# Kernel optimization log

Hardware: AMD Instinct MI355X
Metric: run time of the kernel (lower is better)

The kernel has to match this reference:

```python
import jax, jax.numpy as jnp
import numpy as np

VOCAB, EMB, SEQ, UNITS, BATCH = 10000, 100, 80, 512, 2048


def setup_inputs() -> dict:
    key = jax.random.key(0)
    ks = jax.random.split(key, 8)
    s = 0.05  # param scale for numerical stability
    return {
        "ids": jax.random.randint(ks[0], (BATCH, SEQ), 0, VOCAB, dtype=jnp.int32),
        "emb": jax.random.normal(ks[1], (VOCAB, EMB), jnp.float32) * s,
        "W1": jax.random.normal(ks[2], (EMB, 4 * UNITS), jnp.float32) * s,
        "U1": jax.random.normal(ks[3], (UNITS, 4 * UNITS), jnp.float32) * s,
        "b1": jnp.zeros((4 * UNITS,), jnp.float32),
        "W2": jax.random.normal(ks[4], (UNITS, 4 * UNITS), jnp.float32) * s,
        "U2": jax.random.normal(ks[5], (UNITS, 4 * UNITS), jnp.float32) * s,
        "b2": jnp.zeros((4 * UNITS,), jnp.float32),
        "Wd": jax.random.normal(ks[6], (UNITS, 1), jnp.float32) * s,
        "bd": jnp.zeros((1,), jnp.float32),
    }


def _lstm(x, W, U, b):
    # x: [B,T,D]; Keras gate order i,f,g,o; returns (all h [B,T,U], last h [B,U])
    B = x.shape[0]
    H = U.shape[0]
    h0 = jnp.zeros((B, H), x.dtype)

    def step(carry, xt):
        h, c = carry
        z = xt @ W + h @ U + b  # [B,4H]
        i, f, g, o = jnp.split(z, 4, axis=-1)
        c = jax.nn.sigmoid(f) * c + jax.nn.sigmoid(i) * jnp.tanh(g)
        h = jax.nn.sigmoid(o) * jnp.tanh(c)
        return (h, c), h

    (hT, _), hs = jax.lax.scan(step, (h0, h0), jnp.swapaxes(x, 0, 1))
    return jnp.swapaxes(hs, 0, 1), hT


def reference(ids, emb, W1, U1, b1, W2, U2, b2, Wd, bd):
    x = emb[ids]                       # [B,T,EMB]
    x, _ = _lstm(x, W1, U1, b1)        # return_sequences=True -> [B,T,U]
    _, h = _lstm(x, W2, U2, b2)        # last hidden state [B,U]
    logits = h @ Wd + bd               # Dense(1) head
    return jax.nn.sigmoid(logits)      # [B,1]
```

## Files before the change

kernel.cpp:

```cpp
#include <hip/hip_runtime.h>
#include <hip/hip_bf16.h>
#include <math.h>

#define BATCH 2048
#define SEQ   80
#define EMBD  100
#define HU    512
#define NG    2048

typedef short bf16x8 __attribute__((ext_vector_type(8)));
typedef float f32x4  __attribute__((ext_vector_type(4)));

#define AS1(p) ((const __attribute__((address_space(1))) void*)(p))
#define AS3(p) ((__attribute__((address_space(3))) void*)(p))

__device__ __forceinline__ float sigm(float x){ return 1.f/(1.f+__expf(-x)); }


__global__ __launch_bounds__(256) void prep_emb(const float* __restrict__ emb,
                                                __hip_bfloat16* __restrict__ embp)
{
    int idx = blockIdx.x*256 + threadIdx.x;
    int row = idx >> 7, k = idx & 127;
    float v = (k < EMBD) ? emb[row*EMBD + k] : 0.f;
    embp[idx] = __float2bfloat16(v);
}

__global__ __launch_bounds__(256) void prep_wt(
    const float* __restrict__ W1, const float* __restrict__ U1, const float* __restrict__ b1,
    const float* __restrict__ W2, const float* __restrict__ U2, const float* __restrict__ b2,
    __hip_bfloat16* __restrict__ wt1, __hip_bfloat16* __restrict__ wt2,
    float* __restrict__ bp1, float* __restrict__ bp2)
{
    const int n = blockIdx.x;
    const int u = n >> 2, g = n & 3, col = g*HU + u;
    if (blockIdx.y == 0) {
        for (int k = threadIdx.x; k < 640; k += 256) {
            float v = (k < EMBD) ? W1[k*NG + col] : ((k < 128) ? 0.f : U1[(k-128)*NG + col]);
            wt1[n*640 + k] = __float2bfloat16(v);
        }
        if (threadIdx.x == 0) bp1[n] = b1[col];
    } else {
        for (int k = threadIdx.x; k < 1024; k += 256) {
            float v = (k < HU) ? W2[k*NG + col] : U2[(k-HU)*NG + col];
            wt2[n*1024 + k] = __float2bfloat16(v);
        }
        if (threadIdx.x == 0) bp2[n] = b2[col];
    }
}

__global__ __launch_bounds__(512, 4) void round_k(
    const int* __restrict__ ids, const int r,
    const __hip_bfloat16* __restrict__ embp,
    const __hip_bfloat16* __restrict__ wt1, const float* __restrict__ bp1,
    const __hip_bfloat16* __restrict__ wt2, const float* __restrict__ bp2,
    const __hip_bfloat16* __restrict__ h1prev, __hip_bfloat16* __restrict__ h1out,
    const __hip_bfloat16* __restrict__ h2prev, __hip_bfloat16* __restrict__ h2out,
    float* __restrict__ c1, float* __restrict__ c2,
    const int mode)
{
    __shared__ unsigned short As[2][128*64];
    __shared__ unsigned short Bs[2][128*64];

    const int tid  = threadIdx.x;
    const int w    = tid >> 6;
    const int lane = tid & 63;
    const int wM   = w >> 1;
    const int wN   = w & 1;
    const int m0   = blockIdx.y * 128;
    const int n0   = blockIdx.x * 128;

    const bool isL1 = (mode == 1) || (mode == 0 && blockIdx.z == 1);
    const int t     = isL1 ? r : (r - 1);
    const int KTOT  = isL1 ? 640 : 1024;
    const int K1P   = isL1 ? 128 : 512;
    const __hip_bfloat16* wt    = isL1 ? wt1 : wt2;
    const float*          bp    = isL1 ? bp1 : bp2;
    float*                cst   = isL1 ? c1  : c2;
    const __hip_bfloat16* hprev = isL1 ? h1prev : h2prev;
    const __hip_bfloat16* xs    = h1prev;
    __hip_bfloat16*       hout  = isL1 ? h1out : h2out;

    const int rA = lane & 15;
    const int tq = lane >> 4;

    const int rowA = m0 + w*16 + rA;
    const int rowB = n0 + w*16 + rA;
    int myid = 0;
    if (isL1) myid = ids[rowA*SEQ + t];

    f32x4 acc[2][4];
    #pragma unroll
    for (int mi = 0; mi < 2; ++mi)
        #pragma unroll
        for (int ni = 0; ni < 4; ++ni)
            acc[mi][ni] = (f32x4){0.f,0.f,0.f,0.f};

    auto stage = [&](int kt, int buf){
        const int k0 = kt * 64;
        #pragma unroll
        for (int j = 0; j < 2; ++j) {
            const int kk = k0 + (j*4 + tq)*8;
            const __hip_bfloat16* bx = isL1 ? (embp + (size_t)myid*128)
                                            : (xs + (size_t)rowA*HU);
            const __hip_bfloat16* gpA = (kk < K1P)
                ? (bx + kk)
                : (hprev + (size_t)rowA*HU + (kk - K1P));
            __builtin_amdgcn_global_load_lds(AS1(gpA), AS3(&As[buf][w*1024 + j*512]), 16, 0, 0);
            const __hip_bfloat16* gpB = wt + (size_t)rowB*KTOT + kk;
            __builtin_amdgcn_global_load_lds(AS1(gpB), AS3(&Bs[buf][w*1024 + j*512]), 16, 0, 0);
        }
    };

    stage(0, 0);
    __syncthreads();

    const int NT = KTOT / 64;
    for (int kt = 0; kt < NT; ++kt) {
        const int buf = kt & 1;
        if (kt + 1 < NT) stage(kt + 1, buf ^ 1);

        #pragma unroll
        for (int s = 0; s < 2; ++s) {
            bf16x8 aF[2], bF[4];
            #pragma unroll
            for (int mi = 0; mi < 2; ++mi)
                aF[mi] = *(const bf16x8*)&As[buf][(wM*2+mi)*1024 + (s*4+tq)*128 + rA*8];
            #pragma unroll
            for (int ni = 0; ni < 4; ++ni)
                bF[ni] = *(const bf16x8*)&Bs[buf][(wN*4+ni)*1024 + (s*4+tq)*128 + rA*8];
            #pragma unroll
            for (int mi = 0; mi < 2; ++mi)
                #pragma unroll
                for (int ni = 0; ni < 4; ++ni)
                    acc[mi][ni] = __builtin_amdgcn_mfma_f32_16x16x32_bf16(aF[mi], bF[ni], acc[mi][ni], 0, 0, 0);
        }
        __syncthreads();
    }

    const int gq = lane & 3;
    const bool isT = (gq == 2);
    #pragma unroll
    for (int ni = 0; ni < 4; ++ni) {
        const int n  = n0 + wN*64 + ni*16 + (lane & 15);
        const float bv = bp[n];
        const int u  = n >> 2;
        #pragma unroll
        for (int mi = 0; mi < 2; ++mi) {
            #pragma unroll
            for (int rr = 0; rr < 4; ++rr) {
                const int bM = m0 + wM*32 + mi*16 + (lane >> 4)*4 + rr;
                const float z  = acc[mi][ni][rr] + bv;
                const float zz = isT ? 2.f*z : z;
                const float sg = 1.f/(1.f + __expf(-zz));
                const float act = isT ? fmaf(2.f, sg, -1.f) : sg;
                const float act2 = __shfl_xor(act, 2);
                const float pig  = act * act2;
                const float pig1 = __shfl_xor(pig, 1);
                const float c_old = cst[bM*HU + u];
                const float cn  = fmaf(act, c_old, pig1);
                const float tcn = fmaf(2.f, 1.f/(1.f + __expf(-2.f*cn)), -1.f);
                const float tcn2 = __shfl_xor(tcn, 2);
                const float hv  = act * tcn2;
                if (gq == 1) cst[bM*HU + u] = cn;
                else if (gq == 3) hout[bM*HU + u] = __float2bfloat16(hv);
            }
        }
    }
}

__global__ __launch_bounds__(256) void head_k(const __hip_bfloat16* __restrict__ h2,
    const float* __restrict__ Wd, const float* __restrict__ bd, float* __restrict__ out)
{
    const int b = blockIdx.x*4 + (threadIdx.x >> 6);
    const int lane = threadIdx.x & 63;
    float s = 0.f;
    #pragma unroll
    for (int u = lane; u < HU; u += 64) s += __bfloat162float(h2[b*HU + u]) * Wd[u];
    #pragma unroll
    for (int off = 32; off > 0; off >>= 1) s += __shfl_xor(s, off);
    if (lane == 0) out[b] = 1.f/(1.f + __expf(-(s + bd[0])));
}

extern "C" void kernel_launch(void* const* d_in, const int* in_sizes, int n_in,
                              void* d_out, int out_size, void* d_ws, size_t ws_size,
                              hipStream_t stream)
{
    const int*   ids = (const int*)  d_in[0];
    const float* emb = (const float*)d_in[1];
    const float* W1  = (const float*)d_in[2];
    const float* U1  = (const float*)d_in[3];
    const float* b1  = (const float*)d_in[4];
    const float* W2  = (const float*)d_in[5];
    const float* U2  = (const float*)d_in[6];
    const float* b2  = (const float*)d_in[7];
    const float* Wd  = (const float*)d_in[8];
    const float* bd  = (const float*)d_in[9];
    float* out = (float*)d_out;

    char* p = (char*)d_ws;
    __hip_bfloat16* embp = (__hip_bfloat16*)p; p += (size_t)10000*128*2;
    __hip_bfloat16* wt1  = (__hip_bfloat16*)p; p += (size_t)2048*640*2;
    __hip_bfloat16* wt2  = (__hip_bfloat16*)p; p += (size_t)2048*1024*2;
    float* bp1 = (float*)p; p += 2048*4;
    float* bp2 = (float*)p; p += 2048*4;

    char* state = p;
    const size_t HS = (size_t)BATCH*HU;
    __hip_bfloat16* h1[2]; __hip_bfloat16* h2[2];
    h1[0] = (__hip_bfloat16*)p; p += HS*2;
    h1[1] = (__hip_bfloat16*)p; p += HS*2;
    h2[0] = (__hip_bfloat16*)p; p += HS*2;
    h2[1] = (__hip_bfloat16*)p; p += HS*2;
    float* c1 = (float*)p; p += HS*4;
    float* c2 = (float*)p; p += HS*4;

    hipMemsetAsync(state, 0, HS*(4*2 + 2*4), stream);

    prep_emb<<<10000*128/256, 256, 0, stream>>>(emb, embp);
    prep_wt<<<dim3(2048,2), 256, 0, stream>>>(W1,U1,b1,W2,U2,b2, wt1,wt2,bp1,bp2);

    for (int r = 0; r <= SEQ; ++r) {
        const int mode = (r == 0) ? 1 : ((r == SEQ) ? 2 : 0);
        dim3 g(16, 16, (mode == 0) ? 2 : 1);
        const int cur = r & 1, prv = cur ^ 1;
        round_k<<<g, 512, 0, stream>>>(ids, r, embp, wt1, bp1, wt2, bp2,
                                       h1[prv], h1[cur], h2[prv], h2[cur], c1, c2, mode);
    }
    head_k<<<BATCH/4, 256, 0, stream>>>(h2[0], Wd, bd, out);
}
```

Baseline: 3.200 ms.

## Fuse all LSTM time steps into one persistent kernel with a grid barrier

Replaces the 81 per-step kernel launches with a single persistent kernel of 256 blocks. Each block runs the layer-1 step and then the layer-2 step for its tile, and a global atomic barrier separates time steps. The cell state now lives in LDS for the whole sequence instead of being read and written in global memory every step. This removes launch overhead and the cell-state traffic. In exchange it relies on all 256 blocks being resident at once for the barrier to work, and it runs the two layers one after the other inside each block instead of as separate blocks in parallel.

```diff
diff --git a/kernel.cpp b/kernel.cpp
--- a/kernel.cpp
+++ b/kernel.cpp
@@ -7,14 +7,13 @@
 #define EMBD  100
 #define HU    512
 #define NG    2048
+#define NBLK  256
 
 typedef short bf16x8 __attribute__((ext_vector_type(8)));
 typedef float f32x4  __attribute__((ext_vector_type(4)));
 
 #define AS1(p) ((const __attribute__((address_space(1))) void*)(p))
 #define AS3(p) ((__attribute__((address_space(3))) void*)(p))
-
-__device__ __forceinline__ float sigm(float x){ return 1.f/(1.f+__expf(-x)); }
 
 
 __global__ __launch_bounds__(256) void prep_emb(const float* __restrict__ emb,
@@ -49,45 +48,51 @@
     }
 }
 
-__global__ __launch_bounds__(512, 4) void round_k(
-    const int* __restrict__ ids, const int r,
-    const __hip_bfloat16* __restrict__ embp,
-    const __hip_bfloat16* __restrict__ wt1, const float* __restrict__ bp1,
-    const __hip_bfloat16* __restrict__ wt2, const float* __restrict__ bp2,
-    const __hip_bfloat16* __restrict__ h1prev, __hip_bfloat16* __restrict__ h1out,
-    const __hip_bfloat16* __restrict__ h2prev, __hip_bfloat16* __restrict__ h2out,
-    float* __restrict__ c1, float* __restrict__ c2,
-    const int mode)
-{
-    __shared__ unsigned short As[2][128*64];
-    __shared__ unsigned short Bs[2][128*64];
-
+__device__ __forceinline__ void gbar(unsigned* cnt, unsigned* gen)
+{
+    __syncthreads();
+    if (threadIdx.x == 0) {
+        __threadfence();
+        unsigned g = __hip_atomic_load(gen, __ATOMIC_RELAXED, __HIP_MEMORY_SCOPE_AGENT);
+        unsigned a = __hip_atomic_fetch_add(cnt, 1u, __ATOMIC_ACQ_REL, __HIP_MEMORY_SCOPE_AGENT);
+        if (a == NBLK - 1u) {
+            __hip_atomic_store(cnt, 0u, __ATOMIC_RELAXED, __HIP_MEMORY_SCOPE_AGENT);
+            __hip_atomic_fetch_add(gen, 1u, __ATOMIC_ACQ_REL, __HIP_MEMORY_SCOPE_AGENT);
+        } else {
+            while (__hip_atomic_load(gen, __ATOMIC_RELAXED, __HIP_MEMORY_SCOPE_AGENT) == g)
+                __builtin_amdgcn_s_sleep(2);
+        }
+        __threadfence();
+    }
+    __syncthreads();
+}
+
+template<int KTOT, int K1P, bool GATHER>
+__device__ __forceinline__ void layer_step(
+    const int* __restrict__ ids, const int t,
+    const __hip_bfloat16* __restrict__ xs,
+    const __hip_bfloat16* __restrict__ hprev,
+    const __hip_bfloat16* __restrict__ wt,
+    const float* __restrict__ bp,
+    float* __restrict__ csl,
+    __hip_bfloat16* __restrict__ hout,
+    unsigned short* As0, unsigned short* As1,
+    unsigned short* Bs0, unsigned short* Bs1,
+    const int m0, const int n0)
+{
     const int tid  = threadIdx.x;
     const int w    = tid >> 6;
     const int lane = tid & 63;
     const int wM   = w >> 1;
     const int wN   = w & 1;
-    const int m0   = blockIdx.y * 128;
-    const int n0   = blockIdx.x * 128;
-
-    const bool isL1 = (mode == 1) || (mode == 0 && blockIdx.z == 1);
-    const int t     = isL1 ? r : (r - 1);
-    const int KTOT  = isL1 ? 640 : 1024;
-    const int K1P   = isL1 ? 128 : 512;
-    const __hip_bfloat16* wt    = isL1 ? wt1 : wt2;
-    const float*          bp    = isL1 ? bp1 : bp2;
-    float*                cst   = isL1 ? c1  : c2;
-    const __hip_bfloat16* hprev = isL1 ? h1prev : h2prev;
-    const __hip_bfloat16* xs    = h1prev;
-    __hip_bfloat16*       hout  = isL1 ? h1out : h2out;
 
     const int rA = lane & 15;
     const int tq = lane >> 4;
-
     const int rowA = m0 + w*16 + rA;
     const int rowB = n0 + w*16 + rA;
-    int myid = 0;
-    if (isL1) myid = ids[rowA*SEQ + t];
+
+    const __hip_bfloat16* bx = GATHER ? (xs + (size_t)ids[rowA*SEQ + t]*128)
+                                      : (xs + (size_t)rowA*HU);
 
     f32x4 acc[2][4];
     #pragma unroll
@@ -97,27 +102,29 @@
             acc[mi][ni] = (f32x4){0.f,0.f,0.f,0.f};
 
     auto stage = [&](int kt, int buf){
+        unsigned short* Ad = (buf ? As1 : As0) + w*1024;
+        unsigned short* Bd = (buf ? Bs1 : Bs0) + w*1024;
         const int k0 = kt * 64;
         #pragma unroll
         for (int j = 0; j < 2; ++j) {
             const int kk = k0 + (j*4 + tq)*8;
-            const __hip_bfloat16* bx = isL1 ? (embp + (size_t)myid*128)
-                                            : (xs + (size_t)rowA*HU);
             const __hip_bfloat16* gpA = (kk < K1P)
                 ? (bx + kk)
                 : (hprev + (size_t)rowA*HU + (kk - K1P));
-            __builtin_amdgcn_global_load_lds(AS1(gpA), AS3(&As[buf][w*1024 + j*512]), 16, 0, 0);
+            __builtin_amdgcn_global_load_lds(AS1(gpA), AS3(Ad + j*512), 16, 0, 0);
             const __hip_bfloat16* gpB = wt + (size_t)rowB*KTOT + kk;
-            __builtin_amdgcn_global_load_lds(AS1(gpB), AS3(&Bs[buf][w*1024 + j*512]), 16, 0, 0);
+            __builtin_amdgcn_global_load_lds(AS1(gpB), AS3(Bd + j*512), 16, 0, 0);
         }
     };
 
     stage(0, 0);
     __syncthreads();
 
-    const int NT = KTOT / 64;
+    constexpr int NT = KTOT / 64;
     for (int kt = 0; kt < NT; ++kt) {
         const int buf = kt & 1;
+        const unsigned short* Ab = buf ? As1 : As0;
+        const unsigned short* Bb = buf ? Bs1 : Bs0;
         if (kt + 1 < NT) stage(kt + 1, buf ^ 1);
 
         #pragma unroll
@@ -125,10 +132,10 @@
             bf16x8 aF[2], bF[4];
             #pragma unroll
             for (int mi = 0; mi < 2; ++mi)
-                aF[mi] = *(const bf16x8*)&As[buf][(wM*2+mi)*1024 + (s*4+tq)*128 + rA*8];
+                aF[mi] = *(const bf16x8*)&Ab[(wM*2+mi)*1024 + (s*4+tq)*128 + rA*8];
             #pragma unroll
             for (int ni = 0; ni < 4; ++ni)
-                bF[ni] = *(const bf16x8*)&Bs[buf][(wN*4+ni)*1024 + (s*4+tq)*128 + rA*8];
+                bF[ni] = *(const bf16x8*)&Bb[(wN*4+ni)*1024 + (s*4+tq)*128 + rA*8];
             #pragma unroll
             for (int mi = 0; mi < 2; ++mi)
                 #pragma unroll
@@ -142,14 +149,16 @@
     const bool isT = (gq == 2);
     #pragma unroll
     for (int ni = 0; ni < 4; ++ni) {
-        const int n  = n0 + wN*64 + ni*16 + (lane & 15);
+        const int nl = wN*64 + ni*16 + (lane & 15);
+        const int n  = n0 + nl;
         const float bv = bp[n];
-        const int u  = n >> 2;
+        const int ug  = n >> 2;
+        const int ul  = nl >> 2;
         #pragma unroll
         for (int mi = 0; mi < 2; ++mi) {
             #pragma unroll
             for (int rr = 0; rr < 4; ++rr) {
-                const int bM = m0 + wM*32 + mi*16 + (lane >> 4)*4 + rr;
+                const int rowl = wM*32 + mi*16 + (lane >> 4)*4 + rr;
                 const float z  = acc[mi][ni][rr] + bv;
                 const float zz = isT ? 2.f*z : z;
                 const float sg = 1.f/(1.f + __expf(-zz));
@@ -157,15 +166,55 @@
                 const float act2 = __shfl_xor(act, 2);
                 const float pig  = act * act2;
                 const float pig1 = __shfl_xor(pig, 1);
-                const float c_old = cst[bM*HU + u];
+                const float c_old = csl[rowl*33 + ul];
                 const float cn  = fmaf(act, c_old, pig1);
                 const float tcn = fmaf(2.f, 1.f/(1.f + __expf(-2.f*cn)), -1.f);
                 const float tcn2 = __shfl_xor(tcn, 2);
                 const float hv  = act * tcn2;
-                if (gq == 1) cst[bM*HU + u] = cn;
-                else if (gq == 3) hout[bM*HU + u] = __float2bfloat16(hv);
+                if (gq == 1) csl[rowl*33 + ul] = cn;
+                else if (gq == 3) hout[(size_t)(m0 + rowl)*HU + ug] = __float2bfloat16(hv);
             }
         }
+    }
+}
+
+__global__ __launch_bounds__(512, 2) void lstm_persist(
+    const int* __restrict__ ids,
+    const __hip_bfloat16* __restrict__ embp,
+    const __hip_bfloat16* __restrict__ wt1, const float* __restrict__ bp1,
+    const __hip_bfloat16* __restrict__ wt2, const float* __restrict__ bp2,
+    __hip_bfloat16* h1a, __hip_bfloat16* h1b,
+    __hip_bfloat16* h2a, __hip_bfloat16* h2b,
+    unsigned* cnt, unsigned* gen)
+{
+    __shared__ unsigned short As[2][8192];
+    __shared__ unsigned short Bs[2][8192];
+    __shared__ float cs1[128*33];
+    __shared__ float cs2[128*33];
+
+    const int bid = blockIdx.x;
+    const int uB  = (bid & 7)*2 + ((bid >> 3) & 1);
+    const int rB  = bid >> 4;
+    const int m0  = rB * 128;
+    const int n0  = uB * 128;
+
+    for (int i = threadIdx.x; i < 128*33; i += 512) { cs1[i] = 0.f; cs2[i] = 0.f; }
+
+    for (int r = 0; r <= SEQ; ++r) {
+        const int ip = (r - 1) & 1;
+        const int ic = r & 1;
+        const __hip_bfloat16* h1p = ip ? h1b : h1a;
+        __hip_bfloat16*       h1c = ic ? h1b : h1a;
+        const __hip_bfloat16* h2c = ic ? h2b : h2a;
+        __hip_bfloat16*       h2p = ip ? h2b : h2a;
+
+        if (r < SEQ)
+            layer_step<640,128,true>(ids, r, embp, h1p, wt1, bp1, cs1, h1c,
+                                     &As[0][0], &As[1][0], &Bs[0][0], &Bs[1][0], m0, n0);
+        if (r >= 1)
+            layer_step<1024,512,false>(nullptr, 0, h1p, h2c, wt2, bp2, cs2, h2p,
+                                     &As[0][0], &As[1][0], &Bs[0][0], &Bs[1][0], m0, n0);
+        gbar(cnt, gen);
     }
 }
 
@@ -198,34 +247,26 @@
     const float* bd  = (const float*)d_in[9];
     float* out = (float*)d_out;
 
+    const size_t HS = (size_t)BATCH*HU;
     char* p = (char*)d_ws;
-    __hip_bfloat16* embp = (__hip_bfloat16*)p; p += (size_t)10000*128*2;
-    __hip_bfloat16* wt1  = (__hip_bfloat16*)p; p += (size_t)2048*640*2;
-    __hip_bfloat16* wt2  = (__hip_bfloat16*)p; p += (size_t)2048*1024*2;
-    float* bp1 = (float*)p; p += 2048*4;
-    float* bp2 = (float*)p; p += 2048*4;
-
-    char* state = p;
-    const size_t HS = (size_t)BATCH*HU;
-    __hip_bfloat16* h1[2]; __hip_bfloat16* h2[2];
-    h1[0] = (__hip_bfloat16*)p; p += HS*2;
-    h1[1] = (__hip_bfloat16*)p; p += HS*2;
-    h2[0] = (__hip_bfloat16*)p; p += HS*2;
-    h2[1] = (__hip_bfloat16*)p; p += HS*2;
-    float* c1 = (float*)p; p += HS*4;
-    float* c2 = (float*)p; p += HS*4;
-
-    hipMemsetAsync(state, 0, HS*(4*2 + 2*4), stream);
+    unsigned* bar = (unsigned*)p;                    p += 256;
+    __hip_bfloat16* h1a = (__hip_bfloat16*)p;        p += HS*2;
+    __hip_bfloat16* h1b = (__hip_bfloat16*)p;        p += HS*2;
+    __hip_bfloat16* h2a = (__hip_bfloat16*)p;        p += HS*2;
+    __hip_bfloat16* h2b = (__hip_bfloat16*)p;        p += HS*2;
+    __hip_bfloat16* embp = (__hip_bfloat16*)p;       p += (size_t)10000*128*2;
+    __hip_bfloat16* wt1  = (__hip_bfloat16*)p;       p += (size_t)2048*640*2;
+    __hip_bfloat16* wt2  = (__hip_bfloat16*)p;       p += (size_t)2048*1024*2;
+    float* bp1 = (float*)p;                          p += 2048*4;
+    float* bp2 = (float*)p;                          p += 2048*4;
+
+    hipMemsetAsync(d_ws, 0, 256 + 4*HS*2, stream);
 
     prep_emb<<<10000*128/256, 256, 0, stream>>>(emb, embp);
     prep_wt<<<dim3(2048,2), 256, 0, stream>>>(W1,U1,b1,W2,U2,b2, wt1,wt2,bp1,bp2);
 
-    for (int r = 0; r <= SEQ; ++r) {
-        const int mode = (r == 0) ? 1 : ((r == SEQ) ? 2 : 0);
-        dim3 g(16, 16, (mode == 0) ? 2 : 1);
-        const int cur = r & 1, prv = cur ^ 1;
-        round_k<<<g, 512, 0, stream>>>(ids, r, embp, wt1, bp1, wt2, bp2,
-                                       h1[prv], h1[cur], h2[prv], h2[cur], c1, c2, mode);
-    }
-    head_k<<<BATCH/4, 256, 0, stream>>>(h2[0], Wd, bd, out);
-}
+    lstm_persist<<<NBLK, 512, 0, stream>>>(ids, embp, wt1, bp1, wt2, bp2,
+                                           h1a, h1b, h2a, h2b, &bar[0], &bar[1]);
+
+    head_k<<<BATCH/4, 256, 0, stream>>>(h2b, Wd, bd, out);
+}
```

Result: slower. 5.621 ms (+75.7%).

## Replace per-timestep launches with persistent LSTM kernel using grid barrier

Applied to the files above, without the earlier changes.

Replaces the 81 per-round kernel launches with one persistent kernel of 256 blocks that loops over all timesteps and synchronizes through a global atomic barrier. Each block owns a fixed 64-row by 256-gate tile, so the cell state stays in registers and no longer goes through global memory. The h1 row tile is staged once into LDS and reused by both layers, and both layers run back-to-back inside a round. This removes launch overhead and cell-state traffic, but relies on all 256 blocks being co-resident, since the spin barrier would deadlock otherwise. The heavier per-block LDS footprint also reduces occupancy.

```diff
diff --git a/kernel.cpp b/kernel.cpp
--- a/kernel.cpp
+++ b/kernel.cpp
@@ -1,29 +1,26 @@
 #include <hip/hip_runtime.h>
 #include <hip/hip_bf16.h>
-#include <math.h>
 
 #define BATCH 2048
 #define SEQ   80
 #define EMBD  100
 #define HU    512
 #define NG    2048
+#define NBLK  256
 
 typedef short bf16x8 __attribute__((ext_vector_type(8)));
 typedef float f32x4  __attribute__((ext_vector_type(4)));
+typedef int   i32x4  __attribute__((ext_vector_type(4)));
 
 #define AS1(p) ((const __attribute__((address_space(1))) void*)(p))
 #define AS3(p) ((__attribute__((address_space(3))) void*)(p))
 
-__device__ __forceinline__ float sigm(float x){ return 1.f/(1.f+__expf(-x)); }
-
-
 __global__ __launch_bounds__(256) void prep_emb(const float* __restrict__ emb,
                                                 __hip_bfloat16* __restrict__ embp)
 {
     int idx = blockIdx.x*256 + threadIdx.x;
     int row = idx >> 7, k = idx & 127;
-    float v = (k < EMBD) ? emb[row*EMBD + k] : 0.f;
-    embp[idx] = __float2bfloat16(v);
+    embp[idx] = __float2bfloat16(k < EMBD ? emb[row*EMBD + k] : 0.f);
 }
 
 __global__ __launch_bounds__(256) void prep_wt(
@@ -49,123 +46,222 @@
     }
 }
 
-__global__ __launch_bounds__(512, 4) void round_k(
-    const int* __restrict__ ids, const int r,
+__global__ __launch_bounds__(512, 2) void lstm_persist(
+    const int* __restrict__ ids,
     const __hip_bfloat16* __restrict__ embp,
     const __hip_bfloat16* __restrict__ wt1, const float* __restrict__ bp1,
     const __hip_bfloat16* __restrict__ wt2, const float* __restrict__ bp2,
-    const __hip_bfloat16* __restrict__ h1prev, __hip_bfloat16* __restrict__ h1out,
-    const __hip_bfloat16* __restrict__ h2prev, __hip_bfloat16* __restrict__ h2out,
-    float* __restrict__ c1, float* __restrict__ c2,
-    const int mode)
-{
-    __shared__ unsigned short As[2][128*64];
-    __shared__ unsigned short Bs[2][128*64];
-
-    const int tid  = threadIdx.x;
-    const int w    = tid >> 6;
-    const int lane = tid & 63;
-    const int wM   = w >> 1;
-    const int wN   = w & 1;
-    const int m0   = blockIdx.y * 128;
-    const int n0   = blockIdx.x * 128;
-
-    const bool isL1 = (mode == 1) || (mode == 0 && blockIdx.z == 1);
-    const int t     = isL1 ? r : (r - 1);
-    const int KTOT  = isL1 ? 640 : 1024;
-    const int K1P   = isL1 ? 128 : 512;
-    const __hip_bfloat16* wt    = isL1 ? wt1 : wt2;
-    const float*          bp    = isL1 ? bp1 : bp2;
-    float*                cst   = isL1 ? c1  : c2;
-    const __hip_bfloat16* hprev = isL1 ? h1prev : h2prev;
-    const __hip_bfloat16* xs    = h1prev;
-    __hip_bfloat16*       hout  = isL1 ? h1out : h2out;
-
-    const int rA = lane & 15;
-    const int tq = lane >> 4;
-
-    const int rowA = m0 + w*16 + rA;
-    const int rowB = n0 + w*16 + rA;
-    int myid = 0;
-    if (isL1) myid = ids[rowA*SEQ + t];
-
+    __hip_bfloat16* __restrict__ h1a, __hip_bfloat16* __restrict__ h1b,
+    __hip_bfloat16* __restrict__ h2a, __hip_bfloat16* __restrict__ h2b,
+    unsigned long long* bar)
+{
+    __shared__ __align__(16) unsigned short hx[64*520];
+    __shared__ __align__(16) unsigned short Bs[2][16384];
+    __shared__ __align__(16) unsigned short sb[2][4096];
+
+    const int tid = threadIdx.x;
+    const int w = tid >> 6, lane = tid & 63;
+    const int l15 = lane & 15, tq = lane >> 4;
+    const int wM = w >> 2, wN = w & 3;
+    const int uB = blockIdx.x & 7, rB = blockIdx.x >> 3;
+    const int m0 = rB * 64, n0 = uB * 256;
+
+    float c1r[4][2][4] = {};
+    float c2r[4][2][4] = {};
     f32x4 acc[2][4];
-    #pragma unroll
-    for (int mi = 0; mi < 2; ++mi)
+
+    auto zacc = [&](){
+        #pragma unroll
+        for (int mi = 0; mi < 2; ++mi)
+            #pragma unroll
+            for (int ni = 0; ni < 4; ++ni)
+                acc[mi][ni] = (f32x4){0.f,0.f,0.f,0.f};
+    };
+
+    auto stageB = [&](const __hip_bfloat16* wt, int KTOT, int kt, unsigned short* Bd){
+        const int k0 = kt * 64;
+        #pragma unroll
+        for (int cc = 0; cc < 2; ++cc) {
+            const int chunk = w*2 + cc;
+            #pragma unroll
+            for (int j = 0; j < 2; ++j) {
+                const __hip_bfloat16* gp = wt + (size_t)(n0 + chunk*16 + l15)*KTOT
+                                              + k0 + (j*4 + tq)*8;
+                __builtin_amdgcn_global_load_lds(AS1(gp), AS3(Bd + chunk*1024 + j*512), 16, 0, 0);
+            }
+        }
+    };
+
+    auto afragS = [&](const unsigned short* S, int s, int mi) -> bf16x8 {
+        return *(const bf16x8*)&S[(wM*2 + mi)*1024 + (s*4 + tq)*128 + l15*8];
+    };
+    auto afragH = [&](int kb, int s, int mi) -> bf16x8 {
+        const int row = wM*32 + mi*16 + l15;
+        const int kp  = kb + s*32 + tq*8;
+        return *(const bf16x8*)((const char*)hx + row*1040 + kp*2);
+    };
+    auto mma2 = [&](bf16x8 a0, bf16x8 a1, const unsigned short* Bb, int s){
+        bf16x8 bF[4];
         #pragma unroll
         for (int ni = 0; ni < 4; ++ni)
-            acc[mi][ni] = (f32x4){0.f,0.f,0.f,0.f};
-
-    auto stage = [&](int kt, int buf){
-        const int k0 = kt * 64;
-        #pragma unroll
-        for (int j = 0; j < 2; ++j) {
-            const int kk = k0 + (j*4 + tq)*8;
-            const __hip_bfloat16* bx = isL1 ? (embp + (size_t)myid*128)
-                                            : (xs + (size_t)rowA*HU);
-            const __hip_bfloat16* gpA = (kk < K1P)
-                ? (bx + kk)
-                : (hprev + (size_t)rowA*HU + (kk - K1P));
-            __builtin_amdgcn_global_load_lds(AS1(gpA), AS3(&As[buf][w*1024 + j*512]), 16, 0, 0);
-            const __hip_bfloat16* gpB = wt + (size_t)rowB*KTOT + kk;
-            __builtin_amdgcn_global_load_lds(AS1(gpB), AS3(&Bs[buf][w*1024 + j*512]), 16, 0, 0);
-        }
-    };
-
-    stage(0, 0);
-    __syncthreads();
-
-    const int NT = KTOT / 64;
-    for (int kt = 0; kt < NT; ++kt) {
-        const int buf = kt & 1;
-        if (kt + 1 < NT) stage(kt + 1, buf ^ 1);
-
-        #pragma unroll
-        for (int s = 0; s < 2; ++s) {
-            bf16x8 aF[2], bF[4];
-            #pragma unroll
-            for (int mi = 0; mi < 2; ++mi)
-                aF[mi] = *(const bf16x8*)&As[buf][(wM*2+mi)*1024 + (s*4+tq)*128 + rA*8];
-            #pragma unroll
-            for (int ni = 0; ni < 4; ++ni)
-                bF[ni] = *(const bf16x8*)&Bs[buf][(wN*4+ni)*1024 + (s*4+tq)*128 + rA*8];
-            #pragma unroll
-            for (int mi = 0; mi < 2; ++mi)
+            bF[ni] = *(const bf16x8*)&Bb[(wN*4 + ni)*1024 + (s*4 + tq)*128 + l15*8];
+        #pragma unroll
+        for (int ni = 0; ni < 4; ++ni) {
+            acc[0][ni] = __builtin_amdgcn_mfma_f32_16x16x32_bf16(a0, bF[ni], acc[0][ni], 0, 0, 0);
+            acc[1][ni] = __builtin_amdgcn_mfma_f32_16x16x32_bf16(a1, bF[ni], acc[1][ni], 0, 0, 0);
+        }
+    };
+
+    auto sbwrite = [&](unsigned short* S, i32x4 v){
+        const int row = tid >> 3, t8 = tid & 7;
+        *(i32x4*)((char*)S + ((row >> 4)*1024 + t8*128 + (row & 15)*8)*2) = v;
+    };
+    auto hxwrite = [&](i32x4* hr){
+        #pragma unroll
+        for (int t = 0; t < 8; ++t)
+            *(i32x4*)((char*)hx + (t*8 + (tid >> 6))*1040 + (tid & 63)*16) = hr[t];
+    };
+
+    auto epilogue = [&](const float* bp, float (&cr)[4][2][4], __hip_bfloat16* hdst){
+        const int gq = lane & 3;
+        const bool isT = (gq == 2);
+        unsigned short* hs = &sb[0][0];
+        #pragma unroll
+        for (int ni = 0; ni < 4; ++ni) {
+            const int nl = wN*64 + ni*16 + l15;
+            const float bv = bp[n0 + nl];
+            const int ul = nl >> 2;
+            #pragma unroll
+            for (int mi = 0; mi < 2; ++mi) {
                 #pragma unroll
-                for (int ni = 0; ni < 4; ++ni)
-                    acc[mi][ni] = __builtin_amdgcn_mfma_f32_16x16x32_bf16(aF[mi], bF[ni], acc[mi][ni], 0, 0, 0);
+                for (int rr = 0; rr < 4; ++rr) {
+                    const int rowl = wM*32 + mi*16 + tq*4 + rr;
+                    const float z  = acc[mi][ni][rr] + bv;
+                    const float zz = isT ? 2.f*z : z;
+                    const float sg = 1.f/(1.f + __expf(-zz));
+                    const float act = isT ? fmaf(2.f, sg, -1.f) : sg;
+                    const float act2 = __shfl_xor(act, 2);
+                    const float pig  = act * act2;
+                    const float pig1 = __shfl_xor(pig, 1);
+                    const float cn  = fmaf(act, cr[ni][mi][rr], pig1);
+                    const float tcn = fmaf(2.f, 1.f/(1.f + __expf(-2.f*cn)), -1.f);
+                    const float tcn2 = __shfl_xor(tcn, 2);
+                    const float hv  = act * tcn2;
+                    if (gq == 1) cr[ni][mi][rr] = cn;
+                    if (gq == 3) {
+                        __hip_bfloat16 hb = __float2bfloat16(hv);
+                        hs[rowl*72 + ul] = *(unsigned short*)&hb;
+                    }
+                }
+            }
         }
         __syncthreads();
-    }
-
-    const int gq = lane & 3;
-    const bool isT = (gq == 2);
-    #pragma unroll
-    for (int ni = 0; ni < 4; ++ni) {
-        const int n  = n0 + wN*64 + ni*16 + (lane & 15);
-        const float bv = bp[n];
-        const int u  = n >> 2;
-        #pragma unroll
-        for (int mi = 0; mi < 2; ++mi) {
-            #pragma unroll
-            for (int rr = 0; rr < 4; ++rr) {
-                const int bM = m0 + wM*32 + mi*16 + (lane >> 4)*4 + rr;
-                const float z  = acc[mi][ni][rr] + bv;
-                const float zz = isT ? 2.f*z : z;
-                const float sg = 1.f/(1.f + __expf(-zz));
-                const float act = isT ? fmaf(2.f, sg, -1.f) : sg;
-                const float act2 = __shfl_xor(act, 2);
-                const float pig  = act * act2;
-                const float pig1 = __shfl_xor(pig, 1);
-                const float c_old = cst[bM*HU + u];
-                const float cn  = fmaf(act, c_old, pig1);
-                const float tcn = fmaf(2.f, 1.f/(1.f + __expf(-2.f*cn)), -1.f);
-                const float tcn2 = __shfl_xor(tcn, 2);
-                const float hv  = act * tcn2;
-                if (gq == 1) cst[bM*HU + u] = cn;
-                else if (gq == 3) hout[bM*HU + u] = __float2bfloat16(hv);
-            }
-        }
+        const int row = tid >> 3, ch = tid & 7;
+        i32x4 v = *(const i32x4*)((const char*)hs + row*144 + ch*16);
+        *(volatile i32x4*)(hdst + (size_t)(m0 + row)*HU + uB*64 + ch*8) = v;
+        __syncthreads();
+    };
+
+    auto gbar = [&](){
+        asm volatile("s_waitcnt vmcnt(0)" ::: "memory");
+        __syncthreads();
+        if (tid == 0) {
+            unsigned long long old = __hip_atomic_fetch_add(bar, 1ull,
+                                        __ATOMIC_RELAXED, __HIP_MEMORY_SCOPE_AGENT);
+            unsigned g = (unsigned)(old >> 32);
+            if ((unsigned)(old & 0xffffffffull) == NBLK - 1u) {
+                __hip_atomic_fetch_add(bar, (1ull << 32) - (unsigned long long)NBLK,
+                                       __ATOMIC_RELAXED, __HIP_MEMORY_SCOPE_AGENT);
+            } else {
+                while ((unsigned)(__hip_atomic_load(bar, __ATOMIC_RELAXED,
+                                        __HIP_MEMORY_SCOPE_AGENT) >> 32) == g)
+                    __builtin_amdgcn_s_sleep(8);
+            }
+        }
+        __syncthreads();
+        asm volatile("" ::: "memory");
+    };
+
+    for (int r = 0; r <= SEQ; ++r) {
+        const int ip = (r - 1) & 1, ic = r & 1;
+        const __hip_bfloat16* h1p = ip ? h1b : h1a;
+        __hip_bfloat16*       h1c = ic ? h1b : h1a;
+        const __hip_bfloat16* h2c = ic ? h2b : h2a;
+        __hip_bfloat16*       h2p = ip ? h2b : h2a;
+
+        i32x4 hreg[8];
+        #pragma unroll
+        for (int t = 0; t < 8; ++t)
+            hreg[t] = *(const volatile i32x4*)(h1p + (size_t)(m0 + t*8 + (tid >> 6))*HU
+                                                   + (tid & 63)*8);
+        i32x4 h2g[8];
+        if (r >= 1) {
+            #pragma unroll
+            for (int j = 0; j < 8; ++j)
+                h2g[j] = *(const volatile i32x4*)(h2c + (size_t)(m0 + (tid >> 3))*HU
+                                                      + j*64 + (tid & 7)*8);
+        }
+
+        if (r < SEQ) {
+            const int myid = ids[(m0 + (tid >> 3))*SEQ + r];
+            const __hip_bfloat16* erow = embp + (size_t)myid*128 + (tid & 7)*8;
+            i32x4 e0 = *(const i32x4*)(erow);
+            i32x4 e1 = *(const i32x4*)(erow + 64);
+            zacc();
+            stageB(wt1, 640, 0, &Bs[0][0]);
+            sbwrite(&sb[0][0], e0);
+            __syncthreads();
+            stageB(wt1, 640, 1, &Bs[1][0]);
+            sbwrite(&sb[1][0], e1);
+            #pragma unroll
+            for (int s = 0; s < 2; ++s)
+                mma2(afragS(&sb[0][0], s, 0), afragS(&sb[0][0], s, 1), &Bs[0][0], s);
+            __syncthreads();
+            stageB(wt1, 640, 2, &Bs[0][0]);
+            hxwrite(hreg);
+            #pragma unroll
+            for (int s = 0; s < 2; ++s)
+                mma2(afragS(&sb[1][0], s, 0), afragS(&sb[1][0], s, 1), &Bs[1][0], s);
+            __syncthreads();
+            #pragma unroll
+            for (int kt = 2; kt < 10; ++kt) {
+                if (kt < 9) stageB(wt1, 640, kt + 1, &Bs[(kt + 1) & 1][0]);
+                const int kb = (kt - 2)*64;
+                #pragma unroll
+                for (int s = 0; s < 2; ++s)
+                    mma2(afragH(kb, s, 0), afragH(kb, s, 1), &Bs[kt & 1][0], s);
+                __syncthreads();
+            }
+            epilogue(bp1, c1r, h1c);
+        } else {
+            hxwrite(hreg);
+            __syncthreads();
+        }
+
+        if (r >= 1) {
+            zacc();
+            stageB(wt2, 1024, 0, &Bs[0][0]);
+            __syncthreads();
+            #pragma unroll
+            for (int kt = 0; kt < 16; ++kt) {
+                if (kt < 15) stageB(wt2, 1024, kt + 1, &Bs[(kt + 1) & 1][0]);
+                if (kt >= 7 && kt < 15) sbwrite(&sb[(kt + 1) & 1][0], h2g[kt - 7]);
+                if (kt < 8) {
+                    const int kb = kt*64;
+                    #pragma unroll
+                    for (int s = 0; s < 2; ++s)
+                        mma2(afragH(kb, s, 0), afragH(kb, s, 1), &Bs[kt & 1][0], s);
+                } else {
+                    #pragma unroll
+                    for (int s = 0; s < 2; ++s)
+                        mma2(afragS(&sb[kt & 1][0], s, 0), afragS(&sb[kt & 1][0], s, 1),
+                             &Bs[kt & 1][0], s);
+                }
+                __syncthreads();
+            }
+            epilogue(bp2, c2r, h2p);
+        }
+        gbar();
     }
 }
 
@@ -198,34 +294,26 @@
     const float* bd  = (const float*)d_in[9];
     float* out = (float*)d_out;
 
+    const size_t HS = (size_t)BATCH*HU;
     char* p = (char*)d_ws;
-    __hip_bfloat16* embp = (__hip_bfloat16*)p; p += (size_t)10000*128*2;
-    __hip_bfloat16* wt1  = (__hip_bfloat16*)p; p += (size_t)2048*640*2;
-    __hip_bfloat16* wt2  = (__hip_bfloat16*)p; p += (size_t)2048*1024*2;
-    float* bp1 = (float*)p; p += 2048*4;
-    float* bp2 = (float*)p; p += 2048*4;
-
-    char* state = p;
-    const size_t HS = (size_t)BATCH*HU;
-    __hip_bfloat16* h1[2]; __hip_bfloat16* h2[2];
-    h1[0] = (__hip_bfloat16*)p; p += HS*2;
-    h1[1] = (__hip_bfloat16*)p; p += HS*2;
-    h2[0] = (__hip_bfloat16*)p; p += HS*2;
-    h2[1] = (__hip_bfloat16*)p; p += HS*2;
-    float* c1 = (float*)p; p += HS*4;
-    float* c2 = (float*)p; p += HS*4;
-
-    hipMemsetAsync(state, 0, HS*(4*2 + 2*4), stream);
+    unsigned long long* bar = (unsigned long long*)p;  p += 256;
+    __hip_bfloat16* h1a = (__hip_bfloat16*)p;          p += HS*2;
+    __hip_bfloat16* h1b = (__hip_bfloat16*)p;          p += HS*2;
+    __hip_bfloat16* h2a = (__hip_bfloat16*)p;          p += HS*2;
+    __hip_bfloat16* h2b = (__hip_bfloat16*)p;          p += HS*2;
+    __hip_bfloat16* embp = (__hip_bfloat16*)p;         p += (size_t)10000*128*2;
+    __hip_bfloat16* wt1  = (__hip_bfloat16*)p;         p += (size_t)2048*640*2;
+    __hip_bfloat16* wt2  = (__hip_bfloat16*)p;         p += (size_t)2048*1024*2;
+    float* bp1 = (float*)p;                            p += 2048*4;
+    float* bp2 = (float*)p;                            p += 2048*4;
+
+    hipMemsetAsync(d_ws, 0, 256 + 4*HS*2, stream);
 
     prep_emb<<<10000*128/256, 256, 0, stream>>>(emb, embp);
     prep_wt<<<dim3(2048,2), 256, 0, stream>>>(W1,U1,b1,W2,U2,b2, wt1,wt2,bp1,bp2);
 
-    for (int r = 0; r <= SEQ; ++r) {
-        const int mode = (r == 0) ? 1 : ((r == SEQ) ? 2 : 0);
-        dim3 g(16, 16, (mode == 0) ? 2 : 1);
-        const int cur = r & 1, prv = cur ^ 1;
-        round_k<<<g, 512, 0, stream>>>(ids, r, embp, wt1, bp1, wt2, bp2,
-                                       h1[prv], h1[cur], h2[prv], h2[cur], c1, c2, mode);
-    }
-    head_k<<<BATCH/4, 256, 0, stream>>>(h2[0], Wd, bd, out);
-}
+    lstm_persist<<<NBLK, 512, 0, stream>>>(ids, embp, wt1, bp1, wt2, bp2,
+                                           h1a, h1b, h2a, h2b, bar);
+
+    head_k<<<BATCH/4, 256, 0, stream>>>(h2b, Wd, bd, out);
+}
```

New measurement: 6.562 ms. +105.0%, slower.
